# Kernel optimization log

Hardware: AMD Instinct MI355X
Metric: run time of the kernel (lower is better)

Reference implementation:

```python
import jax, jax.numpy as jnp
import numpy as np

EMBED = 1024
HEADS = 16
HEAD_DIM = EMBED // HEADS
EPS = 1e-5


def setup_inputs() -> dict:
    key = jax.random.key(0)
    ks = jax.random.split(key, 5)
    s = 1.0 / np.sqrt(EMBED)
    return {
        "x": jax.random.normal(ks[0], (2, 2048, EMBED), dtype=jnp.float32),
        "Wq": jax.random.normal(ks[1], (EMBED, EMBED), dtype=jnp.float32) * s,
        "Wk": jax.random.normal(ks[2], (EMBED, EMBED), dtype=jnp.float32) * s,
        "Wv": jax.random.normal(ks[3], (EMBED, EMBED), dtype=jnp.float32) * s,
        "Wout": jax.random.normal(ks[4], (EMBED, EMBED), dtype=jnp.float32) * s,
        "gamma": jnp.ones((EMBED,), dtype=jnp.float32),
        "beta": jnp.zeros((EMBED,), dtype=jnp.float32),
    }


def reference(x, Wq, Wk, Wv, Wout, gamma, beta):
    B, S, E = x.shape
    # nn.Linear(bias=False): y = x @ W.T; weight stored as [out, in]
    q = (x @ Wq.T).reshape(B, S, HEADS, HEAD_DIM)
    k = (x @ Wk.T).reshape(B, S, HEADS, HEAD_DIM)
    v = (x @ Wv.T).reshape(B, S, HEADS, HEAD_DIM)
    scale = 1.0 / jnp.sqrt(jnp.float32(HEAD_DIM)).astype(x.dtype)
    scores = jnp.einsum("bqhd,bkhd->bhqk", q, k) * scale  # [B,H,S,S]
    probs = jax.nn.softmax(scores, axis=-1)
    attn = jnp.einsum("bhqk,bkhd->bqhd", probs, v).reshape(B, S, E)
    out = attn @ Wout.T
    y = out + x
    mu = jnp.mean(y, axis=-1, keepdims=True)
    var = jnp.var(y, axis=-1, keepdims=True)
    return (y - mu) * jax.lax.rsqrt(var + EPS) * gamma + beta
```

## Files before the change

kernel.cpp:

```cpp
#include <hip/hip_runtime.h>
#include <hip/hip_bf16.h>
#include <cstdint>
#include <cstddef>

#define SEQ   2048
#define BATCH 2
#define NROWS 4096
#define EMB   1024
#define NHEAD 16
#define HD    64
#define QBLK  64
#define KVBLK 64

typedef __attribute__((ext_vector_type(8))) short bf16x8;
typedef __attribute__((ext_vector_type(4))) float f32x4;
typedef __hip_bfloat16 bf16_t;

__device__ __forceinline__ int swz(int row, int cb) { return cb ^ ((row & 7) << 4); }
__device__ __forceinline__ float max3f(float a, float b, float c) {
  return fmaxf(fmaxf(a, b), c);
}

__global__ __launch_bounds__(256) void cast_f32_to_bf16(const float* __restrict__ in,
                                                        bf16_t* __restrict__ out, int n4) {
  int i = blockIdx.x * 256 + threadIdx.x;
  if (i >= n4) return;
  float4 v = reinterpret_cast<const float4*>(in)[i];
  union { ushort4 u; bf16_t h[4]; } o;
  o.h[0] = __float2bfloat16(v.x);
  o.h[1] = __float2bfloat16(v.y);
  o.h[2] = __float2bfloat16(v.z);
  o.h[3] = __float2bfloat16(v.w);
  reinterpret_cast<ushort4*>(out)[i] = o.u;
}

__global__ __launch_bounds__(256) void cast4_w(const float* __restrict__ a,
                                               const float* __restrict__ b,
                                               const float* __restrict__ c,
                                               const float* __restrict__ d,
                                               bf16_t* __restrict__ oa, bf16_t* __restrict__ ob,
                                               bf16_t* __restrict__ oc, bf16_t* __restrict__ od,
                                               int n4) {
  const int z = blockIdx.z;
  const float* in = (z == 0) ? a : (z == 1) ? b : (z == 2) ? c : d;
  bf16_t* out = (z == 0) ? oa : (z == 1) ? ob : (z == 2) ? oc : od;
  int i = blockIdx.x * 256 + threadIdx.x;
  if (i >= n4) return;
  float4 v = reinterpret_cast<const float4*>(in)[i];
  union { ushort4 u; bf16_t h[4]; } o;
  o.h[0] = __float2bfloat16(v.x);
  o.h[1] = __float2bfloat16(v.y);
  o.h[2] = __float2bfloat16(v.z);
  o.h[3] = __float2bfloat16(v.w);
  reinterpret_cast<ushort4*>(out)[i] = o.u;
}

template <int MODE>
__device__ __forceinline__ void gemm128_body(const bf16_t* __restrict__ A,
                                             const bf16_t* __restrict__ W,
                                             bf16_t* __restrict__ Ob,
                                             float* __restrict__ Of,
                                             const float* __restrict__ Res) {
  __shared__ __align__(16) bf16_t As[128 * 32];
  __shared__ __align__(16) bf16_t Bs[128 * 32];
  const int tid = threadIdx.x;
  const int lane = tid & 63;
  const int wv = tid >> 6;
  const int wm = wv >> 1, wn = wv & 1;
  const int brow = blockIdx.y * 128;
  const int bcol = blockIdx.x * 128;
  const int lr = lane & 15, lg = lane >> 4;

  f32x4 acc[4][4] = {};

  auto* As3 = (__attribute__((address_space(3))) char*)As;
  auto* Bs3 = (__attribute__((address_space(3))) char*)Bs;

  for (int k0 = 0; k0 < EMB; k0 += 32) {
    __syncthreads();
#pragma unroll
    for (int i = 0; i < 2; ++i) {
      const int chunk = i * 256 + tid;
      const int row = chunk >> 2;
      const int kc = (chunk & 3) * 8;
      const bf16_t* ga = A + (size_t)(brow + row) * EMB + k0 + kc;
      const bf16_t* gb = W + (size_t)(bcol + row) * EMB + k0 + kc;
      __builtin_amdgcn_global_load_lds((const __attribute__((address_space(1))) void*)ga,
                                       (__attribute__((address_space(3))) void*)(As3 + chunk * 16),
                                       16, 0, 0);
      __builtin_amdgcn_global_load_lds((const __attribute__((address_space(1))) void*)gb,
                                       (__attribute__((address_space(3))) void*)(Bs3 + chunk * 16),
                                       16, 0, 0);
    }
    __syncthreads();

    bf16x8 af[4], bfr[4];
#pragma unroll
    for (int m = 0; m < 4; ++m)
      af[m] = *reinterpret_cast<const bf16x8*>(&As[(wm * 64 + m * 16 + lr) * 32 + lg * 8]);
#pragma unroll
    for (int n = 0; n < 4; ++n)
      bfr[n] = *reinterpret_cast<const bf16x8*>(&Bs[(wn * 64 + n * 16 + lr) * 32 + lg * 8]);
#pragma unroll
    for (int m = 0; m < 4; ++m)
#pragma unroll
      for (int n = 0; n < 4; ++n)
        acc[m][n] = __builtin_amdgcn_mfma_f32_16x16x32_bf16(af[m], bfr[n], acc[m][n], 0, 0, 0);
  }

  const int r0 = brow + wm * 64;
  const int c0 = bcol + wn * 64;
#pragma unroll
  for (int m = 0; m < 4; ++m)
#pragma unroll
    for (int n = 0; n < 4; ++n) {
      if (MODE == 2) {
        const int row0 = r0 + m * 16 + lg * 4;
        const int col = c0 + n * 16 + lr;
        const size_t vt_row = (size_t)(row0 >> 11) * 1024 + col;
        const int s = row0 & 2047;
        union { uint2 u2; bf16_t h[4]; } pu;
#pragma unroll
        for (int r = 0; r < 4; ++r) pu.h[r] = __float2bfloat16(acc[m][n][r]);
        *reinterpret_cast<uint2*>(Ob + vt_row * SEQ + s) = pu.u2;
      } else {
#pragma unroll
        for (int r = 0; r < 4; ++r) {
          const int row = r0 + m * 16 + lg * 4 + r;
          const int col = c0 + n * 16 + lr;
          const size_t idx = (size_t)row * EMB + col;
          if (MODE == 0) Ob[idx] = __float2bfloat16(acc[m][n][r]);
          else Of[idx] = acc[m][n][r] + Res[idx];
        }
      }
    }
}

__global__ __launch_bounds__(256) void gemm_qkv(const bf16_t* __restrict__ X,
                                                const bf16_t* __restrict__ Wq,
                                                const bf16_t* __restrict__ Wk,
                                                const bf16_t* __restrict__ Wv,
                                                bf16_t* __restrict__ Q,
                                                bf16_t* __restrict__ K,
                                                bf16_t* __restrict__ Vt) {
  if (blockIdx.z == 0)      gemm128_body<0>(X, Wq, Q, nullptr, nullptr);
  else if (blockIdx.z == 1) gemm128_body<0>(X, Wk, K, nullptr, nullptr);
  else                      gemm128_body<2>(X, Wv, Vt, nullptr, nullptr);
}

__global__ __launch_bounds__(256) void gemm_out(const bf16_t* __restrict__ Attn,
                                                const bf16_t* __restrict__ Wo,
                                                float* __restrict__ Y,
                                                const float* __restrict__ X) {
  gemm128_body<1>(Attn, Wo, nullptr, Y, X);
}

__global__ __launch_bounds__(256) void attn_kernel(const bf16_t* __restrict__ Q,
                                                   const bf16_t* __restrict__ K,
                                                   const bf16_t* __restrict__ Vt,
                                                   bf16_t* __restrict__ Oout) {
  __shared__ __align__(16) bf16_t Ks[2][KVBLK * 64];
  __shared__ __align__(16) bf16_t Vs[2][64 * KVBLK];
  __shared__ __align__(16) bf16_t Pl[4][16 * 64];

  const int tid = threadIdx.x;
  const int lane = tid & 63;
  const int wv = tid >> 6;
  const int lr = lane & 15, lg = lane >> 4;

  const int f = blockIdx.x + 32 * blockIdx.y + 512 * blockIdx.z;
  const int w = (f & 7) * 128 + (f >> 3);
  const int qb = w & 31;
  const int h = (w >> 5) & 15;
  const int b = w >> 9;

  const size_t baseRow = (size_t)b * SEQ;
  const int hoff = h * HD;
  const int q0 = qb * QBLK + wv * 16;

  const float qscale = 0.125f * 1.44269504f;
  bf16x8 qf[2];
#pragma unroll
  for (int kk = 0; kk < 2; ++kk) {
    bf16x8 t = *reinterpret_cast<const bf16x8*>(
        &Q[(baseRow + q0 + lr) * EMB + hoff + kk * 32 + lg * 8]);
    union { bf16x8 v; bf16_t h[8]; } u;
    u.v = t;
#pragma unroll
    for (int e = 0; e < 8; ++e)
      u.h[e] = __float2bfloat16(__bfloat162float(u.h[e]) * qscale);
    qf[kk] = u.v;
  }

  f32x4 o[4] = {};
  float mrow = -1e30f, lrow = 0.f;

  auto* Ks3 = (__attribute__((address_space(3))) char*)&Ks[0][0];
  auto* Vs3 = (__attribute__((address_space(3))) char*)&Vs[0][0];

  const int srow = tid >> 3;
  const int scb = swz(srow, (tid & 7) * 16) >> 1;
  const bf16_t* kp = K + (baseRow + srow) * EMB + hoff + scb;
  const bf16_t* vp = Vt + ((size_t)(b * 1024 + hoff) + srow) * SEQ + scb;

  auto stage = [&](int buf, const bf16_t* kpp, const bf16_t* vpp) {
#pragma unroll
    for (int i = 0; i < 2; ++i) {
      const int c = i * 256 + tid;
      __builtin_amdgcn_global_load_lds(
          (const __attribute__((address_space(1))) void*)(kpp + i * 32 * EMB),
          (__attribute__((address_space(3))) void*)(Ks3 + buf * 8192 + c * 16), 16, 0, 0);
      __builtin_amdgcn_global_load_lds(
          (const __attribute__((address_space(1))) void*)(vpp + i * 32 * SEQ),
          (__attribute__((address_space(3))) void*)(Vs3 + buf * 8192 + c * 16), 16, 0, 0);
    }
  };

  stage(0, kp, vp);
  kp += KVBLK * EMB;
  vp += KVBLK;
  __syncthreads();

  for (int it = 0; it < SEQ / KVBLK; ++it) {
    const int cur = it & 1;
    if (it + 1 < SEQ / KVBLK) {
      stage(cur ^ 1, kp, vp);
      kp += KVBLK * EMB;
      vp += KVBLK;
    }

    const char* Kb = (const char*)Ks + cur * 8192;
    const char* Vb = (const char*)Vs + cur * 8192;

    f32x4 st[4] = {};
    __builtin_amdgcn_s_setprio(1);
#pragma unroll
    for (int t = 0; t < 4; ++t) {
      const int row = t * 16 + lr;
#pragma unroll
      for (int kk = 0; kk < 2; ++kk) {
        bf16x8 kf = *reinterpret_cast<const bf16x8*>(Kb + row * 128 + swz(lr, kk * 64 + lg * 16));
        st[t] = __builtin_amdgcn_mfma_f32_16x16x32_bf16(kf, qf[kk], st[t], 0, 0, 0);
      }
    }
    __builtin_amdgcn_s_setprio(0);

    const float m0 = max3f(st[0][0], st[0][1], st[0][2]);
    const float m1 = max3f(st[0][3], st[1][0], st[1][1]);
    const float m2 = max3f(st[1][2], st[1][3], st[2][0]);
    const float m3 = max3f(st[2][1], st[2][2], st[2][3]);
    const float m4 = max3f(st[3][0], st[3][1], st[3][2]);
    float mx = fmaxf(max3f(m0, m1, m2), max3f(m3, m4, st[3][3]));
    mx = fmaxf(mx, __shfl_xor(mx, 16));
    mx = fmaxf(mx, __shfl_xor(mx, 32));

    if (!__all(mx - mrow <= 8.f)) {
      const float mnew = fmaxf(mrow, mx);
      const float al = __builtin_amdgcn_exp2f(mrow - mnew);
      mrow = mnew;
      lrow *= al;
#pragma unroll
      for (int t = 0; t < 4; ++t)
#pragma unroll
        for (int r = 0; r < 4; ++r) o[t][r] *= al;
    }

    float lsp[4];
#pragma unroll
    for (int t = 0; t < 4; ++t) {
#pragma unroll
      for (int r = 0; r < 4; ++r) st[t][r] = __builtin_amdgcn_exp2f(st[t][r] - mrow);
      lsp[t] = (st[t][0] + st[t][1]) + (st[t][2] + st[t][3]);
    }
    float ls = (lsp[0] + lsp[1]) + (lsp[2] + lsp[3]);
    ls += __shfl_xor(ls, 16);
    ls += __shfl_xor(ls, 32);
    lrow += ls;

    char* Plw = (char*)&Pl[wv][0];
#pragma unroll
    for (int t = 0; t < 4; ++t) {
      uint32_t d0, d1;
      asm("v_cvt_pk_bf16_f32 %0, %1, %2" : "=v"(d0) : "v"(st[t][0]), "v"(st[t][1]));
      asm("v_cvt_pk_bf16_f32 %0, %1, %2" : "=v"(d1) : "v"(st[t][2]), "v"(st[t][3]));
      uint2 u2; u2.x = d0; u2.y = d1;
      *reinterpret_cast<uint2*>(Plw + lr * 128 + swz(lr, t * 32 + lg * 8)) = u2;
    }
    bf16x8 pf[2];
#pragma unroll
    for (int jt = 0; jt < 2; ++jt)
      pf[jt] = *reinterpret_cast<const bf16x8*>(Plw + lr * 128 + swz(lr, jt * 64 + lg * 16));

    __builtin_amdgcn_s_setprio(1);
#pragma unroll
    for (int t = 0; t < 4; ++t) {
      const int row = t * 16 + lr;
#pragma unroll
      for (int jt = 0; jt < 2; ++jt) {
        bf16x8 vf = *reinterpret_cast<const bf16x8*>(Vb + row * 128 + swz(lr, jt * 64 + lg * 16));
        o[t] = __builtin_amdgcn_mfma_f32_16x16x32_bf16(vf, pf[jt], o[t], 0, 0, 0);
      }
    }
    __builtin_amdgcn_s_setprio(0);

    __syncthreads();
  }

  const float inv = 1.f / lrow;
  const size_t orow = (baseRow + q0 + lr) * EMB + hoff;
#pragma unroll
  for (int t = 0; t < 4; ++t) {
    union { uint2 u2; bf16_t h[4]; } pu;
#pragma unroll
    for (int r = 0; r < 4; ++r) pu.h[r] = __float2bfloat16(o[t][r] * inv);
    *reinterpret_cast<uint2*>(Oout + orow + t * 16 + lg * 4) = pu.u2;
  }
}

__global__ __launch_bounds__(256) void ln_kernel(const float* __restrict__ Y,
                                                 const float* __restrict__ gamma,
                                                 const float* __restrict__ beta,
                                                 float* __restrict__ Out) {
  const int row = blockIdx.x;
  const int tid = threadIdx.x;
  const float4 v = reinterpret_cast<const float4*>(Y + (size_t)row * EMB)[tid];
  float s = v.x + v.y + v.z + v.w;
  float s2 = v.x * v.x + v.y * v.y + v.z * v.z + v.w * v.w;
#pragma unroll
  for (int m = 1; m < 64; m <<= 1) {
    s += __shfl_xor(s, m);
    s2 += __shfl_xor(s2, m);
  }
  __shared__ float ws[4], ws2[4];
  const int w = tid >> 6;
  if ((tid & 63) == 0) { ws[w] = s; ws2[w] = s2; }
  __syncthreads();
  s = ws[0] + ws[1] + ws[2] + ws[3];
  s2 = ws2[0] + ws2[1] + ws2[2] + ws2[3];
  const float mu = s * (1.f / EMB);
  const float var = s2 * (1.f / EMB) - mu * mu;
  const float rstd = rsqrtf(var + 1e-5f);
  const float4 g = reinterpret_cast<const float4*>(gamma)[tid];
  const float4 bt = reinterpret_cast<const float4*>(beta)[tid];
  float4 ov;
  ov.x = (v.x - mu) * rstd * g.x + bt.x;
  ov.y = (v.y - mu) * rstd * g.y + bt.y;
  ov.z = (v.z - mu) * rstd * g.z + bt.z;
  ov.w = (v.w - mu) * rstd * g.w + bt.w;
  reinterpret_cast<float4*>(Out + (size_t)row * EMB)[tid] = ov;
}

extern "C" void kernel_launch(void* const* d_in, const int* in_sizes, int n_in,
                              void* d_out, int out_size, void* d_ws, size_t ws_size,
                              hipStream_t stream) {
  const float* x = (const float*)d_in[0];
  const float* Wq = (const float*)d_in[1];
  const float* Wk = (const float*)d_in[2];
  const float* Wv = (const float*)d_in[3];
  const float* Wo = (const float*)d_in[4];
  const float* gamma = (const float*)d_in[5];
  const float* beta = (const float*)d_in[6];
  float* out = (float*)d_out;

  char* p = (char*)d_ws;
  const size_t sz_rows_bf = (size_t)NROWS * EMB * sizeof(bf16_t);
  const size_t sz_w_bf = (size_t)EMB * EMB * sizeof(bf16_t);
  bf16_t* xb = (bf16_t*)p; p += sz_rows_bf;
  bf16_t* wqb = (bf16_t*)p; p += sz_w_bf;
  bf16_t* wkb = (bf16_t*)p; p += sz_w_bf;
  bf16_t* wvb = (bf16_t*)p; p += sz_w_bf;
  bf16_t* wob = (bf16_t*)p; p += sz_w_bf;
  bf16_t* q = (bf16_t*)p; p += sz_rows_bf;
  bf16_t* k = (bf16_t*)p; p += sz_rows_bf;
  bf16_t* vt = (bf16_t*)p; p += sz_rows_bf;
  bf16_t* attn = (bf16_t*)p; p += sz_rows_bf;
  float* y = (float*)q;

  const int n4x = NROWS * EMB / 4;
  const int n4w = EMB * EMB / 4;
  cast_f32_to_bf16<<<n4x / 256, 256, 0, stream>>>(x, xb, n4x);
  cast4_w<<<dim3(n4w / 256, 1, 4), 256, 0, stream>>>(Wq, Wk, Wv, Wo, wqb, wkb, wvb, wob, n4w);

  gemm_qkv<<<dim3(EMB / 128, NROWS / 128, 3), 256, 0, stream>>>(xb, wqb, wkb, wvb, q, k, vt);

  attn_kernel<<<dim3(SEQ / QBLK, NHEAD, BATCH), 256, 0, stream>>>(q, k, vt, attn);

  gemm_out<<<dim3(EMB / 128, NROWS / 128, 1), 256, 0, stream>>>(attn, wob, y, x);

  ln_kernel<<<NROWS, 256, 0, stream>>>(y, gamma, beta, out);
}
```

Before: 140.5 us.

## Switch attention to 32x32x16 MFMA with 128-query blocks and register P transpose

The attention kernel now uses 32x32x16 bf16 MFMA tiles, so each wave handles 32 query rows and each block handles 128 queries, which halves the grid. The softmax probabilities are packed to bf16 and rearranged into the B-operand layout with permlane32 swaps instead of a round trip through LDS. Row max and sum reductions also use the permlane swap. This gives more K/V reuse per LDS load and removes the P staging traffic, at the cost of more registers per thread and fewer blocks, which may lower occupancy.

```diff
diff --git a/kernel.cpp b/kernel.cpp
--- a/kernel.cpp
+++ b/kernel.cpp
@@ -9,16 +9,36 @@
 #define EMB   1024
 #define NHEAD 16
 #define HD    64
-#define QBLK  64
 #define KVBLK 64
 
 typedef __attribute__((ext_vector_type(8))) short bf16x8;
 typedef __attribute__((ext_vector_type(4))) float f32x4;
+typedef __attribute__((ext_vector_type(16))) float f32x16;
+typedef __attribute__((ext_vector_type(2))) int i32x2;
 typedef __hip_bfloat16 bf16_t;
 
 __device__ __forceinline__ int swz(int row, int cb) { return cb ^ ((row & 7) << 4); }
-__device__ __forceinline__ float max3f(float a, float b, float c) {
-  return fmaxf(fmaxf(a, b), c);
+
+__device__ __forceinline__ void plswap(int a, int b, int& ra, int& rb) {
+#if __has_builtin(__builtin_amdgcn_permlane32_swap)
+  i32x2 r = __builtin_amdgcn_permlane32_swap(a, b, false, false);
+  ra = r[0]; rb = r[1];
+#else
+  const int pa = __shfl_xor(a, 32), pb = __shfl_xor(b, 32);
+  const bool lo = (threadIdx.x & 63) < 32;
+  ra = lo ? a : pb;
+  rb = lo ? pa : b;
+#endif
+}
+__device__ __forceinline__ float pairmax32(float v) {
+  int r0, r1;
+  plswap(__float_as_int(v), __float_as_int(v), r0, r1);
+  return fmaxf(__int_as_float(r0), __int_as_float(r1));
+}
+__device__ __forceinline__ float pairsum32(float v) {
+  int r0, r1;
+  plswap(__float_as_int(v), __float_as_int(v), r0, r1);
+  return __int_as_float(r0) + __int_as_float(r1);
 }
 
 __global__ __launch_bounds__(256) void cast_f32_to_bf16(const float* __restrict__ in,
@@ -161,38 +181,38 @@
                                                    bf16_t* __restrict__ Oout) {
   __shared__ __align__(16) bf16_t Ks[2][KVBLK * 64];
   __shared__ __align__(16) bf16_t Vs[2][64 * KVBLK];
-  __shared__ __align__(16) bf16_t Pl[4][16 * 64];
 
   const int tid = threadIdx.x;
   const int lane = tid & 63;
   const int wv = tid >> 6;
-  const int lr = lane & 15, lg = lane >> 4;
-
-  const int f = blockIdx.x + 32 * blockIdx.y + 512 * blockIdx.z;
-  const int w = (f & 7) * 128 + (f >> 3);
-  const int qb = w & 31;
-  const int h = (w >> 5) & 15;
-  const int b = w >> 9;
+  const int lq = lane & 31;
+  const int lh = lane >> 5;
+
+  const int f = blockIdx.x + 16 * blockIdx.y + 256 * blockIdx.z;
+  const int w = (f & 7) * 64 + (f >> 3);
+  const int qb = w & 15;
+  const int h = (w >> 4) & 15;
+  const int b = w >> 8;
 
   const size_t baseRow = (size_t)b * SEQ;
   const int hoff = h * HD;
-  const int q0 = qb * QBLK + wv * 16;
+  const int q0 = qb * 128 + wv * 32;
 
   const float qscale = 0.125f * 1.44269504f;
-  bf16x8 qf[2];
-#pragma unroll
-  for (int kk = 0; kk < 2; ++kk) {
+  bf16x8 qf[4];
+#pragma unroll
+  for (int ks = 0; ks < 4; ++ks) {
     bf16x8 t = *reinterpret_cast<const bf16x8*>(
-        &Q[(baseRow + q0 + lr) * EMB + hoff + kk * 32 + lg * 8]);
+        &Q[(baseRow + q0 + lq) * EMB + hoff + ks * 16 + lh * 8]);
     union { bf16x8 v; bf16_t h[8]; } u;
     u.v = t;
 #pragma unroll
     for (int e = 0; e < 8; ++e)
       u.h[e] = __float2bfloat16(__bfloat162float(u.h[e]) * qscale);
-    qf[kk] = u.v;
+    qf[ks] = u.v;
   }
 
-  f32x4 o[4] = {};
+  f32x16 o[2] = {};
   float mrow = -1e30f, lrow = 0.f;
 
   auto* Ks3 = (__attribute__((address_space(3))) char*)&Ks[0][0];
@@ -232,27 +252,25 @@
     const char* Kb = (const char*)Ks + cur * 8192;
     const char* Vb = (const char*)Vs + cur * 8192;
 
-    f32x4 st[4] = {};
+    f32x16 st[2] = {};
     __builtin_amdgcn_s_setprio(1);
 #pragma unroll
-    for (int t = 0; t < 4; ++t) {
-      const int row = t * 16 + lr;
-#pragma unroll
-      for (int kk = 0; kk < 2; ++kk) {
-        bf16x8 kf = *reinterpret_cast<const bf16x8*>(Kb + row * 128 + swz(lr, kk * 64 + lg * 16));
-        st[t] = __builtin_amdgcn_mfma_f32_16x16x32_bf16(kf, qf[kk], st[t], 0, 0, 0);
+    for (int jh = 0; jh < 2; ++jh) {
+      const int row = jh * 32 + lq;
+#pragma unroll
+      for (int ks = 0; ks < 4; ++ks) {
+        bf16x8 kf = *reinterpret_cast<const bf16x8*>(Kb + row * 128 + swz(lq, ks * 32 + lh * 16));
+        st[jh] = __builtin_amdgcn_mfma_f32_32x32x16_bf16(kf, qf[ks], st[jh], 0, 0, 0);
       }
     }
     __builtin_amdgcn_s_setprio(0);
 
-    const float m0 = max3f(st[0][0], st[0][1], st[0][2]);
-    const float m1 = max3f(st[0][3], st[1][0], st[1][1]);
-    const float m2 = max3f(st[1][2], st[1][3], st[2][0]);
-    const float m3 = max3f(st[2][1], st[2][2], st[2][3]);
-    const float m4 = max3f(st[3][0], st[3][1], st[3][2]);
-    float mx = fmaxf(max3f(m0, m1, m2), max3f(m3, m4, st[3][3]));
-    mx = fmaxf(mx, __shfl_xor(mx, 16));
-    mx = fmaxf(mx, __shfl_xor(mx, 32));
+    float mx = -1e30f;
+#pragma unroll
+    for (int jh = 0; jh < 2; ++jh)
+#pragma unroll
+      for (int r = 0; r < 16; ++r) mx = fmaxf(mx, st[jh][r]);
+    mx = pairmax32(mx);
 
     if (!__all(mx - mrow <= 8.f)) {
       const float mnew = fmaxf(mrow, mx);
@@ -260,45 +278,50 @@
       mrow = mnew;
       lrow *= al;
 #pragma unroll
-      for (int t = 0; t < 4; ++t)
-#pragma unroll
-        for (int r = 0; r < 4; ++r) o[t][r] *= al;
-    }
-
-    float lsp[4];
-#pragma unroll
-    for (int t = 0; t < 4; ++t) {
-#pragma unroll
-      for (int r = 0; r < 4; ++r) st[t][r] = __builtin_amdgcn_exp2f(st[t][r] - mrow);
-      lsp[t] = (st[t][0] + st[t][1]) + (st[t][2] + st[t][3]);
-    }
-    float ls = (lsp[0] + lsp[1]) + (lsp[2] + lsp[3]);
-    ls += __shfl_xor(ls, 16);
-    ls += __shfl_xor(ls, 32);
-    lrow += ls;
-
-    char* Plw = (char*)&Pl[wv][0];
-#pragma unroll
-    for (int t = 0; t < 4; ++t) {
-      uint32_t d0, d1;
-      asm("v_cvt_pk_bf16_f32 %0, %1, %2" : "=v"(d0) : "v"(st[t][0]), "v"(st[t][1]));
-      asm("v_cvt_pk_bf16_f32 %0, %1, %2" : "=v"(d1) : "v"(st[t][2]), "v"(st[t][3]));
-      uint2 u2; u2.x = d0; u2.y = d1;
-      *reinterpret_cast<uint2*>(Plw + lr * 128 + swz(lr, t * 32 + lg * 8)) = u2;
-    }
-    bf16x8 pf[2];
-#pragma unroll
-    for (int jt = 0; jt < 2; ++jt)
-      pf[jt] = *reinterpret_cast<const bf16x8*>(Plw + lr * 128 + swz(lr, jt * 64 + lg * 16));
+      for (int jh = 0; jh < 2; ++jh)
+#pragma unroll
+        for (int r = 0; r < 16; ++r) o[jh][r] *= al;
+    }
+
+    float lsp[2];
+#pragma unroll
+    for (int jh = 0; jh < 2; ++jh) {
+#pragma unroll
+      for (int r = 0; r < 16; ++r) st[jh][r] = __builtin_amdgcn_exp2f(st[jh][r] - mrow);
+      float a0 = (st[jh][0] + st[jh][1]) + (st[jh][2] + st[jh][3]);
+      float a1 = (st[jh][4] + st[jh][5]) + (st[jh][6] + st[jh][7]);
+      float a2 = (st[jh][8] + st[jh][9]) + (st[jh][10] + st[jh][11]);
+      float a3 = (st[jh][12] + st[jh][13]) + (st[jh][14] + st[jh][15]);
+      lsp[jh] = (a0 + a1) + (a2 + a3);
+    }
+    lrow += pairsum32(lsp[0] + lsp[1]);
+
+    bf16x8 pb[4];
+#pragma unroll
+    for (int jh = 0; jh < 2; ++jh)
+#pragma unroll
+      for (int sub = 0; sub < 2; ++sub) {
+        int w01, w23, w45, w67;
+        asm("v_cvt_pk_bf16_f32 %0, %1, %2" : "=v"(w01) : "v"(st[jh][sub * 8 + 0]), "v"(st[jh][sub * 8 + 1]));
+        asm("v_cvt_pk_bf16_f32 %0, %1, %2" : "=v"(w23) : "v"(st[jh][sub * 8 + 2]), "v"(st[jh][sub * 8 + 3]));
+        asm("v_cvt_pk_bf16_f32 %0, %1, %2" : "=v"(w45) : "v"(st[jh][sub * 8 + 4]), "v"(st[jh][sub * 8 + 5]));
+        asm("v_cvt_pk_bf16_f32 %0, %1, %2" : "=v"(w67) : "v"(st[jh][sub * 8 + 6]), "v"(st[jh][sub * 8 + 7]));
+        int d0, d1, d2, d3;
+        plswap(w01, w45, d0, d2);
+        plswap(w23, w67, d1, d3);
+        union { int i[4]; bf16x8 v; } u;
+        u.i[0] = d0; u.i[1] = d1; u.i[2] = d2; u.i[3] = d3;
+        pb[jh * 2 + sub] = u.v;
+      }
 
     __builtin_amdgcn_s_setprio(1);
 #pragma unroll
-    for (int t = 0; t < 4; ++t) {
-      const int row = t * 16 + lr;
-#pragma unroll
-      for (int jt = 0; jt < 2; ++jt) {
-        bf16x8 vf = *reinterpret_cast<const bf16x8*>(Vb + row * 128 + swz(lr, jt * 64 + lg * 16));
-        o[t] = __builtin_amdgcn_mfma_f32_16x16x32_bf16(vf, pf[jt], o[t], 0, 0, 0);
+    for (int dh = 0; dh < 2; ++dh) {
+      const int row = dh * 32 + lq;
+#pragma unroll
+      for (int js = 0; js < 4; ++js) {
+        bf16x8 vf = *reinterpret_cast<const bf16x8*>(Vb + row * 128 + swz(lq, js * 32 + lh * 16));
+        o[dh] = __builtin_amdgcn_mfma_f32_32x32x16_bf16(vf, pb[js], o[dh], 0, 0, 0);
       }
     }
     __builtin_amdgcn_s_setprio(0);
@@ -307,14 +330,16 @@
   }
 
   const float inv = 1.f / lrow;
-  const size_t orow = (baseRow + q0 + lr) * EMB + hoff;
-#pragma unroll
-  for (int t = 0; t < 4; ++t) {
-    union { uint2 u2; bf16_t h[4]; } pu;
-#pragma unroll
-    for (int r = 0; r < 4; ++r) pu.h[r] = __float2bfloat16(o[t][r] * inv);
-    *reinterpret_cast<uint2*>(Oout + orow + t * 16 + lg * 4) = pu.u2;
-  }
+  const size_t orow = (baseRow + q0 + lq) * EMB + hoff;
+#pragma unroll
+  for (int dh = 0; dh < 2; ++dh)
+#pragma unroll
+    for (int g = 0; g < 4; ++g) {
+      union { uint2 u2; bf16_t h[4]; } pu;
+#pragma unroll
+      for (int r = 0; r < 4; ++r) pu.h[r] = __float2bfloat16(o[dh][g * 4 + r] * inv);
+      *reinterpret_cast<uint2*>(Oout + orow + dh * 32 + g * 8 + lh * 4) = pu.u2;
+    }
 }
 
 __global__ __launch_bounds__(256) void ln_kernel(const float* __restrict__ Y,
@@ -383,7 +408,7 @@
 
   gemm_qkv<<<dim3(EMB / 128, NROWS / 128, 3), 256, 0, stream>>>(xb, wqb, wkb, wvb, q, k, vt);
 
-  attn_kernel<<<dim3(SEQ / QBLK, NHEAD, BATCH), 256, 0, stream>>>(q, k, vt, attn);
+  attn_kernel<<<dim3(SEQ / 128, NHEAD, BATCH), 256, 0, stream>>>(q, k, vt, attn);
 
   gemm_out<<<dim3(EMB / 128, NROWS / 128, 1), 256, 0, stream>>>(attn, wob, y, x);
 
```

New measurement: 133.9 us. 1.05x faster.
